# Optimization experiments

Measured on AMD Instinct MI355X. Metric: run time of the kernel, lower is better.

## Reference

```python
import jax, jax.numpy as jnp
import numpy as np

N, K, C, H, FF, OUT = 50000, 48, 128, 8, 256, 128
D = C // H  # head dim


def layernorm(x, g, b, eps=1e-5):
    m = jnp.mean(x, axis=-1, keepdims=True)
    v = jnp.mean((x - m) ** 2, axis=-1, keepdims=True)
    return (x - m) * jax.lax.rsqrt(v + eps) * g + b


def setup_inputs() -> dict:
    key = jax.random.key(0)
    ks = jax.random.split(key, 16)
    voxel_features = jax.random.normal(ks[0], (N, C), jnp.float32)
    voxel_coords = jax.random.uniform(ks[1], (N, 3), jnp.float32) * 400.0
    # neighbor indices; values >= N emulate missing neighbors (gather idx < 0 in original)
    raw = jax.random.randint(ks[2], (N, K), 0, N + N // 4)
    key_mask = raw >= N
    key_indices = jnp.where(key_mask, 0, raw).astype(jnp.int32)
    key_indices = key_indices.at[:, 0].set(jnp.arange(N, dtype=jnp.int32))  # self always valid
    key_mask = key_mask.at[:, 0].set(False)
    s = 1.0 / np.sqrt(C)
    params = dict(
        in_proj_w=jax.random.normal(ks[3], (3 * C, C), jnp.float32) * s,
        in_proj_b=jnp.zeros((3 * C,), jnp.float32),
        out_proj_w=jax.random.normal(ks[4], (C, C), jnp.float32) * s,
        out_proj_b=jnp.zeros((C,), jnp.float32),
        k_pos_w=jax.random.normal(ks[5], (C, 3), jnp.float32) * 0.5,
        k_pos_b=jnp.zeros((C,), jnp.float32),
        ln1_g=jnp.ones((C,), jnp.float32), ln1_b=jnp.zeros((C,), jnp.float32),
        ln2_g=jnp.ones((C,), jnp.float32), ln2_b=jnp.zeros((C,), jnp.float32),
        ff1_w=jax.random.normal(ks[6], (FF, C), jnp.float32) * s,
        ff1_b=jnp.zeros((FF,), jnp.float32),
        ff2_w=jax.random.normal(ks[7], (C, FF), jnp.float32) * (1.0 / np.sqrt(FF)),
        ff2_b=jnp.zeros((C,), jnp.float32),
        out_w=jax.random.normal(ks[8], (OUT, C), jnp.float32) * s,
        out_b=jnp.zeros((OUT,), jnp.float32),
        ln3_g=jnp.ones((OUT,), jnp.float32), ln3_b=jnp.zeros((OUT,), jnp.float32),
    )
    return dict(voxel_features=voxel_features, voxel_coords=voxel_coords,
                key_indices=key_indices, key_mask=key_mask, **params)


def reference(voxel_features, voxel_coords, key_indices, key_mask,
              in_proj_w, in_proj_b, out_proj_w, out_proj_b,
              k_pos_w, k_pos_b, ln1_g, ln1_b, ln2_g, ln2_b,
              ff1_w, ff1_b, ff2_w, ff2_b, out_w, out_b, ln3_g, ln3_b):
    # gather neighbor features and coords: [N, K, C] / [N, K, 3]
    key_feats = voxel_features[key_indices]
    rel_coords = voxel_coords[key_indices] - voxel_coords[:, None, :]
    # conv1d(3->C, kernel 1) + ReLU positional embedding
    pos_emb = jax.nn.relu(jnp.einsum('nkt,ct->nkc', rel_coords, k_pos_w) + k_pos_b)
    key_feats = key_feats + pos_emb
    # multi-head attention, query seq_len = 1 per voxel
    wq, wk, wv = in_proj_w[:C], in_proj_w[C:2 * C], in_proj_w[2 * C:]
    bq, bk, bv = in_proj_b[:C], in_proj_b[C:2 * C], in_proj_b[2 * C:]
    q = (voxel_features @ wq.T + bq).reshape(N, H, D)
    k = (jnp.einsum('nkc,ec->nke', key_feats, wk) + bk).reshape(N, K, H, D)
    v = (jnp.einsum('nkc,ec->nke', key_feats, wv) + bv).reshape(N, K, H, D)
    scores = jnp.einsum('nhd,nkhd->nhk', q, k) / np.sqrt(D)
    scores = jnp.where(key_mask[:, None, :], jnp.float32(-1e9), scores)
    attn = jax.nn.softmax(scores, axis=-1)
    ctx = jnp.einsum('nhk,nkhd->nhd', attn, v).reshape(N, C)
    attend = ctx @ out_proj_w.T + out_proj_b
    # residual + norm + FFN + norm
    x = layernorm(voxel_features + attend, ln1_g, ln1_b)
    ff = jax.nn.relu(x @ ff1_w.T + ff1_b) @ ff2_w.T + ff2_b
    x = layernorm(x + ff, ln2_g, ln2_b)
    # output layer: Linear -> LayerNorm -> ReLU
    out = jax.nn.relu(layernorm(x @ out_w.T + out_b, ln3_g, ln3_b))
    return out
```

## Files before the change

kernel.cpp:

```cpp
#include <hip/hip_runtime.h>
#include <stdint.h>

typedef unsigned char u8;
typedef unsigned short us;
typedef unsigned int u32;

#define CDIM  128
#define KNBR  48
#define HEADS 8
#define DHEAD 16
#define FFDIM 256

using bf16x8 = __attribute__((ext_vector_type(8))) short;
using f32x4  = __attribute__((ext_vector_type(4))) float;

__device__ inline float blo32(u32 u) { union { u32 i; float f; } v; v.i = u << 16; return v.f; }
__device__ inline float bhi32(u32 u) { union { u32 i; float f; } v; v.i = u & 0xFFFF0000u; return v.f; }
__device__ inline float bf2f(us u) { union { u32 i; float f; } v; v.i = ((u32)u) << 16; return v.f; }
__device__ inline us f2bf(float x) {
    union { float f; u32 i; } v; v.f = x;
    u32 r = v.i + 0x7FFFu + ((v.i >> 16) & 1u);
    return (us)(r >> 16);
}
__device__ inline u32 cvtpk(float a, float b) {
    u32 r;
    asm("v_cvt_pk_bf16_f32 %0, %1, %2" : "=v"(r) : "v"(a), "v"(b));
    return r;
}

__global__ void k_mask_probe(const u32* __restrict__ mw, int nwords,
                             int* __restrict__ flag)
{
    u32 any = 0;
    for (int j = blockIdx.x * blockDim.x + threadIdx.x; j < nwords;
         j += gridDim.x * blockDim.x)
        any |= mw[j] & 0xFFFFFF00u;
    if (any) atomicOr(flag, 1);
}

__global__ __launch_bounds__(256) void k_wt(
    const float* __restrict__ W, float* __restrict__ WT, int E, int C4)
{
    int i = blockIdx.x * 256 + threadIdx.x;
    if (i < E * C4) {
        int e = i / C4, c4 = i - e * C4;
        float4 v = *(const float4*)(W + (size_t)e * (C4 * 4) + c4 * 4);
        ((float4*)WT)[(size_t)c4 * E + e] = v;
    }
}

__global__ __launch_bounds__(256) void k_wb(
    const float* __restrict__ W, us* __restrict__ WB, int n2)
{
    int i = blockIdx.x * 256 + threadIdx.x;
    if (i < n2) {
        float2 v = *(const float2*)(W + (size_t)i * 2);
        ((u32*)WB)[i] = cvtpk(v.x, v.y);
    }
}

__global__ __launch_bounds__(384) void k_qkv(
    const float* __restrict__ F, const float* __restrict__ WT,
    const float* __restrict__ B,
    float* __restrict__ Q, us* __restrict__ FkB, us* __restrict__ FvB, int N)
{
    __shared__ float xL[8][CDIM];
    int row0 = blockIdx.x * 8;
    int t = threadIdx.x;
    for (int o = t; o < 8 * CDIM; o += 384) {
        int r = o >> 7, c = o & 127;
        int row = row0 + r;
        xL[r][c] = (row < N) ? F[row * CDIM + c] : 0.f;
    }
    __syncthreads();

    int e = t;
    const float4* WT4 = (const float4*)WT;
    float acc[8] = {0.f,0.f,0.f,0.f,0.f,0.f,0.f,0.f};
    #pragma unroll 8
    for (int c4 = 0; c4 < CDIM / 4; ++c4) {
        float4 w = WT4[c4 * 384 + e];
        #pragma unroll
        for (int r = 0; r < 8; ++r) {
            const float* x = &xL[r][c4 * 4];
            acc[r] += x[0]*w.x + x[1]*w.y + x[2]*w.z + x[3]*w.w;
        }
    }
    float bv = B[e];
    if (e < 128) {
        #pragma unroll
        for (int r = 0; r < 8; ++r) {
            int row = row0 + r;
            if (row < N) Q[row * CDIM + e] = acc[r] + bv;
        }
    } else if (e < 256) {
        int eo = e - 128;
        #pragma unroll
        for (int r = 0; r < 8; ++r) {
            int row = row0 + r;
            if (row < N) FkB[(size_t)row * CDIM + eo] = f2bf(acc[r] + bv);
        }
    } else {
        int eo = e - 256;
        #pragma unroll
        for (int r = 0; r < 8; ++r) {
            int row = row0 + r;
            if (row < N) FvB[(size_t)row * CDIM + eo] = f2bf(acc[r] + bv);
        }
    }
}

__global__ __launch_bounds__(256, 6) void k_attn(
    const float* __restrict__ coords, const int* __restrict__ kidx,
    const u8* __restrict__ kmask_u8, const int* __restrict__ kmask_i32,
    const int* __restrict__ maskflag,
    const float* __restrict__ Q, const us* __restrict__ FkB,
    const us* __restrict__ FvB,
    const float* __restrict__ wk, const float* __restrict__ wv,
    const float* __restrict__ kpw, const float* __restrict__ kpb,
    float* __restrict__ CTX)
{
    __shared__ __align__(16) u8 SM[14656];
    us*    qwH   = (us*)(SM);
    us*    qwL   = (us*)(SM + 2176);
    float* scL   = (float*)(SM + 4352);
    float* Ql    = (float*)(SM + 6016);
    float* rel   = (float*)(SM + 6528);
    float* kpw0S = (float*)(SM + 7104);
    float* kpw1S = (float*)(SM + 7616);
    float* kpw2S = (float*)(SM + 8128);
    float* kpbS  = (float*)(SM + 8640);
    int*   idxl  = (int*)  (SM + 9152);
    u8*    mskl  = (u8*)   (SM + 9344);
    float* Pb    = (float*)(SM + 9408);
    float* pc    = (float*)(SM + 13632);

    int n = blockIdx.x;
    int t = threadIdx.x;
    int w = t >> 6, lane = t & 63;

    if (t < KNBR) {
        int idx = kidx[n * KNBR + t];
        idxl[t] = idx;
        mskl[t] = maskflag[0] ? kmask_u8[n * KNBR + t]
                              : (u8)kmask_i32[n * KNBR + t];
        rel[t * 3 + 0] = coords[idx * 3 + 0] - coords[n * 3 + 0];
        rel[t * 3 + 1] = coords[idx * 3 + 1] - coords[n * 3 + 1];
        rel[t * 3 + 2] = coords[idx * 3 + 2] - coords[n * 3 + 2];
    }
    if (t < 128) {
        kpw0S[t] = kpw[t * 3 + 0];
        kpw1S[t] = kpw[t * 3 + 1];
        kpw2S[t] = kpw[t * 3 + 2];
        kpbS[t]  = kpb[t];
    } else {
        Ql[t - 128] = Q[n * CDIM + (t - 128)];
    }
    __syncthreads();

    {
        int h = t >> 5, c4 = t & 31;
        const float* qh = Ql + h * DHEAD;
        float a0=0.f, a1=0.f, a2=0.f, a3=0.f;
        #pragma unroll
        for (int d = 0; d < DHEAD; ++d) {
            float q = qh[d];
            float4 wr = *(const float4*)(wk + (size_t)(h * DHEAD + d) * CDIM + c4 * 4);
            a0 += q * wr.x; a1 += q * wr.y; a2 += q * wr.z; a3 += q * wr.w;
        }
        uint2 ph, pl;
        ph.x = cvtpk(a0, a1);
        ph.y = cvtpk(a2, a3);
        pl.x = cvtpk(a0 - blo32(ph.x), a1 - bhi32(ph.x));
        pl.y = cvtpk(a2 - blo32(ph.y), a3 - bhi32(ph.y));
        *(uint2*)&qwH[h * 136 + c4 * 4] = ph;
        *(uint2*)&qwL[h * 136 + c4 * 4] = pl;
    }

    if (w == 3) {
        #pragma unroll
        for (int i = 0; i < 6; ++i) {
            int o = lane * 6 + i;
            int k = o >> 3, h = o & 7;
            const float* qh = Ql + h * DHEAD;
            const uint4* fk = (const uint4*)(FkB + (size_t)idxl[k] * CDIM + h * DHEAD);
            uint4 fa = fk[0], fb = fk[1];
            float s = qh[0]*blo32(fa.x) + qh[1]*bhi32(fa.x)
                    + qh[2]*blo32(fa.y) + qh[3]*bhi32(fa.y)
                    + qh[4]*blo32(fa.z) + qh[5]*bhi32(fa.z)
                    + qh[6]*blo32(fa.w) + qh[7]*bhi32(fa.w)
                    + qh[8]*blo32(fb.x) + qh[9]*bhi32(fb.x)
                    + qh[10]*blo32(fb.y) + qh[11]*bhi32(fb.y)
                    + qh[12]*blo32(fb.z) + qh[13]*bhi32(fb.z)
                    + qh[14]*blo32(fb.w) + qh[15]*bhi32(fb.w);
            scL[h * 52 + k] = s;
        }
    }
    __syncthreads();

    union U8 { bf16x8 v; u32 wd[4]; };

    if (w < 3) {
        f32x4 acc = {0.f, 0.f, 0.f, 0.f};
        int kk = w * 16 + (lane & 15);
        int cb0 = (lane >> 4) * 8;
        int arow = lane & 15;
        bool aval = arow < 8;
        bf16x8 zz = {0,0,0,0,0,0,0,0};
        float r0 = rel[kk * 3], r1 = rel[kk * 3 + 1], r2 = rel[kk * 3 + 2];
        #pragma unroll
        for (int s = 0; s < 4; ++s) {
            int cb = cb0 + s * 32;
            float4 x0 = *(const float4*)&kpw0S[cb], x1 = *(const float4*)&kpw0S[cb + 4];
            float4 y0 = *(const float4*)&kpw1S[cb], y1 = *(const float4*)&kpw1S[cb + 4];
            float4 z0 = *(const float4*)&kpw2S[cb], z1 = *(const float4*)&kpw2S[cb + 4];
            float4 b0 = *(const float4*)&kpbS[cb],  b1 = *(const float4*)&kpbS[cb + 4];
            float p[8];
            p[0] = fmaxf(b0.x + r0*x0.x + r1*y0.x + r2*z0.x, 0.f);
            p[1] = fmaxf(b0.y + r0*x0.y + r1*y0.y + r2*z0.y, 0.f);
            p[2] = fmaxf(b0.z + r0*x0.z + r1*y0.z + r2*z0.z, 0.f);
            p[3] = fmaxf(b0.w + r0*x0.w + r1*y0.w + r2*z0.w, 0.f);
            p[4] = fmaxf(b1.x + r0*x1.x + r1*y1.x + r2*z1.x, 0.f);
            p[5] = fmaxf(b1.y + r0*x1.y + r1*y1.y + r2*z1.y, 0.f);
            p[6] = fmaxf(b1.z + r0*x1.z + r1*y1.z + r2*z1.z, 0.f);
            p[7] = fmaxf(b1.w + r0*x1.w + r1*y1.w + r2*z1.w, 0.f);
            U8 bh, bl;
            #pragma unroll
            for (int j = 0; j < 4; ++j) {
                u32 hh = cvtpk(p[2*j], p[2*j+1]);
                bh.wd[j] = hh;
                bl.wd[j] = cvtpk(p[2*j] - blo32(hh), p[2*j+1] - bhi32(hh));
            }
            int c0 = s * 32 + cb0;
            bf16x8 ah = aval ? *(const bf16x8*)(qwH + arow * 136 + c0) : zz;
            bf16x8 al = aval ? *(const bf16x8*)(qwL + arow * 136 + c0) : zz;
            acc = __builtin_amdgcn_mfma_f32_16x16x32_bf16(ah, bh.v, acc, 0, 0, 0);
            acc = __builtin_amdgcn_mfma_f32_16x16x32_bf16(ah, bl.v, acc, 0, 0, 0);
            acc = __builtin_amdgcn_mfma_f32_16x16x32_bf16(al, bh.v, acc, 0, 0, 0);
        }
        if (lane < 32) {
            int kc = w * 16 + (lane & 15);
            int rb = (lane >> 4) * 4;
            u8 mk = mskl[kc];
            #pragma unroll
            for (int j = 0; j < 4; ++j) {
                int h = rb + j;
                float s = acc[j] + scL[h * 52 + kc];
                scL[h * 52 + kc] = mk ? -1e30f : s * 0.25f;
            }
        }
    }
    __syncthreads();

    {
        int h = t >> 5, l32 = t & 31;
        float* sc = scL + h * 52;
        float v0 = sc[l32];
        float v1 = (l32 < KNBR - 32) ? sc[l32 + 32] : -1e30f;
        float m = fmaxf(v0, v1);
        #pragma unroll
        for (int off = 16; off >= 1; off >>= 1)
            m = fmaxf(m, __shfl_xor(m, off, 32));
        float e0 = __expf(v0 - m);
        float e1 = (l32 < KNBR - 32) ? __expf(v1 - m) : 0.f;
        float s = e0 + e1;
        #pragma unroll
        for (int off = 16; off >= 1; off >>= 1)
            s += __shfl_xor(s, off, 32);
        float inv = 1.f / s;
        sc[l32] = e0 * inv;
        if (l32 < KNBR - 32) sc[l32 + 32] = e1 * inv;
    }
    __syncthreads();

    {
        bf16x8 AH[2], AL[2];
        int arow = lane & 15;
        bool av = arow < 8;
        #pragma unroll
        for (int st = 0; st < 2; ++st) {
            int k0 = (lane >> 4) * 8 + st * 32;
            float pr[8];
            if (av && k0 < KNBR) {
                float4 s0 = *(const float4*)&scL[arow * 52 + k0];
                float4 s1 = *(const float4*)&scL[arow * 52 + k0 + 4];
                pr[0]=s0.x; pr[1]=s0.y; pr[2]=s0.z; pr[3]=s0.w;
                pr[4]=s1.x; pr[5]=s1.y; pr[6]=s1.z; pr[7]=s1.w;
            } else {
                #pragma unroll
                for (int j = 0; j < 8; ++j) pr[j] = 0.f;
            }
            U8 ah, al;
            #pragma unroll
            for (int j = 0; j < 4; ++j) {
                u32 hh = cvtpk(pr[2*j], pr[2*j+1]);
                ah.wd[j] = hh;
                al.wd[j] = cvtpk(pr[2*j] - blo32(hh), pr[2*j+1] - bhi32(hh));
            }
            AH[st] = ah.v; AL[st] = al.v;
        }
        #pragma unroll
        for (int ct = 0; ct < 2; ++ct) {
            int c = w * 32 + ct * 16 + (lane & 15);
            float w0 = kpw0S[c], w1 = kpw1S[c], w2 = kpw2S[c], bb = kpbS[c];
            f32x4 acc = {0.f, 0.f, 0.f, 0.f};
            #pragma unroll
            for (int st = 0; st < 2; ++st) {
                int k0 = (lane >> 4) * 8 + st * 32;
                U8 bh;
                if (k0 < KNBR) {
                    #pragma unroll
                    for (int j = 0; j < 4; ++j) {
                        const float* ra = rel + (k0 + 2*j) * 3;
                        const float* rb = rel + (k0 + 2*j + 1) * 3;
                        float pa = fmaxf(bb + ra[0]*w0 + ra[1]*w1 + ra[2]*w2, 0.f);
                        float pb = fmaxf(bb + rb[0]*w0 + rb[1]*w1 + rb[2]*w2, 0.f);
                        bh.wd[j] = cvtpk(pa, pb);
                    }
                } else {
                    bh.wd[0]=bh.wd[1]=bh.wd[2]=bh.wd[3]=0u;
                }
                acc = __builtin_amdgcn_mfma_f32_16x16x32_bf16(AH[st], bh.v, acc, 0, 0, 0);
                acc = __builtin_amdgcn_mfma_f32_16x16x32_bf16(AL[st], bh.v, acc, 0, 0, 0);
            }
            if (lane < 32) {
                int rb2 = (lane >> 4) * 4;
                #pragma unroll
                for (int j = 0; j < 4; ++j)
                    Pb[(rb2 + j) * 132 + c] = acc[j];
            }
        }
    }
    __syncthreads();

    {
        int c = t & 127, half = t >> 7;
        int h = c >> 4;
        const float* sc = scL + h * 52;
        float accF = 0.f;
        #pragma unroll 4
        for (int kk = 0; kk < 24; ++kk) {
            int k = half * 24 + kk;
            accF += sc[k] * bf2f(FvB[(size_t)idxl[k] * CDIM + c]);
        }
        const float4* wr = (const float4*)(wv + (size_t)c * CDIM) + half * 16;
        const float4* pb4 = (const float4*)(Pb + h * 132) + half * 16;
        #pragma unroll 4
        for (int j = 0; j < 16; ++j) {
            float4 wq = wr[j], p = pb4[j];
            accF += wq.x*p.x + wq.y*p.y + wq.z*p.z + wq.w*p.w;
        }
        pc[half * 128 + c] = accF;
    }
    __syncthreads();
    if (t < CDIM) CTX[n * CDIM + t] = pc[t] + pc[128 + t];
}

__global__ __launch_bounds__(256) void k_proj_ln_m(
    const float* __restrict__ X, const float* __restrict__ RES,
    const us* __restrict__ WB, const float* __restrict__ B,
    const float* __restrict__ G, const float* __restrict__ LB,
    float* __restrict__ OUT, int N, int relu_out)
{
    __shared__ us xB[16 * 136];
    __shared__ float aL[16][CDIM + 4];
    __shared__ float mu[16], rs[16];
    int row0 = blockIdx.x * 16;
    int t = threadIdx.x;
    {
        int r = t >> 4, cb = (t & 15) * 8;
        int row = row0 + r;
        uint4 o = make_uint4(0, 0, 0, 0);
        if (row < N) {
            float4 v0 = *(const float4*)&X[(size_t)row * CDIM + cb];
            float4 v1 = *(const float4*)&X[(size_t)row * CDIM + cb + 4];
            o.x = cvtpk(v0.x, v0.y); o.y = cvtpk(v0.z, v0.w);
            o.z = cvtpk(v1.x, v1.y); o.w = cvtpk(v1.z, v1.w);
        }
        *(uint4*)&xB[r * 136 + cb] = o;
    }
    __syncthreads();

    int w = t >> 6, lane = t & 63;
    int arow = lane & 15, ko = (lane >> 4) * 8;
    bf16x8 afr[4];
    #pragma unroll
    for (int s = 0; s < 4; ++s)
        afr[s] = *(const bf16x8*)&xB[arow * 136 + s * 32 + ko];

    #pragma unroll
    for (int ct = 0; ct < 2; ++ct) {
        int e0 = (w * 2 + ct) * 16;
        f32x4 acc = {0.f, 0.f, 0.f, 0.f};
        #pragma unroll
        for (int s = 0; s < 4; ++s) {
            bf16x8 bfr = *(const bf16x8*)&WB[(size_t)(e0 + arow) * CDIM + s * 32 + ko];
            acc = __builtin_amdgcn_mfma_f32_16x16x32_bf16(afr[s], bfr, acc, 0, 0, 0);
        }
        int e = e0 + arow;
        float bb = B[e];
        #pragma unroll
        for (int jj = 0; jj < 4; ++jj) {
            int r = (lane >> 4) * 4 + jj;
            int row = row0 + r;
            float a = acc[jj] + bb;
            if (RES != nullptr && row < N) a += RES[(size_t)row * CDIM + e];
            aL[r][e] = a;
        }
    }
    __syncthreads();

    {
        int r = t >> 4, j = t & 15;
        float s = 0.f;
        #pragma unroll
        for (int jj = 0; jj < 8; ++jj) s += aL[r][j * 8 + jj];
        #pragma unroll
        for (int off = 8; off >= 1; off >>= 1) s += __shfl_xor(s, off, 16);
        float mean = s * (1.f / 128.f);
        float v = 0.f;
        #pragma unroll
        for (int jj = 0; jj < 8; ++jj) {
            float d = aL[r][j * 8 + jj] - mean; v += d * d;
        }
        #pragma unroll
        for (int off = 8; off >= 1; off >>= 1) v += __shfl_xor(v, off, 16);
        if (j == 0) { mu[r] = mean; rs[r] = rsqrtf(v * (1.f / 128.f) + 1e-5f); }
    }
    __syncthreads();

    for (int o = t; o < 16 * CDIM; o += 256) {
        int r = o >> 7, c = o & 127;
        int row = row0 + r;
        if (row < N) {
            float y = (aL[r][c] - mu[r]) * rs[r] * G[c] + LB[c];
            if (relu_out) y = fmaxf(y, 0.f);
            OUT[row * CDIM + c] = y;
        }
    }
}

__global__ __launch_bounds__(256) void k_ff1_m(
    const float* __restrict__ X, const us* __restrict__ WB,
    const float* __restrict__ B, us* __restrict__ HID, int N)
{
    __shared__ us xB[16 * 136];
    int row0 = blockIdx.x * 16;
    int t = threadIdx.x;
    {
        int r = t >> 4, cb = (t & 15) * 8;
        int row = row0 + r;
        uint4 o = make_uint4(0, 0, 0, 0);
        if (row < N) {
            float4 v0 = *(const float4*)&X[(size_t)row * CDIM + cb];
            float4 v1 = *(const float4*)&X[(size_t)row * CDIM + cb + 4];
            o.x = cvtpk(v0.x, v0.y); o.y = cvtpk(v0.z, v0.w);
            o.z = cvtpk(v1.x, v1.y); o.w = cvtpk(v1.z, v1.w);
        }
        *(uint4*)&xB[r * 136 + cb] = o;
    }
    __syncthreads();

    int w = t >> 6, lane = t & 63;
    int arow = lane & 15, ko = (lane >> 4) * 8;
    bf16x8 afr[4];
    #pragma unroll
    for (int s = 0; s < 4; ++s)
        afr[s] = *(const bf16x8*)&xB[arow * 136 + s * 32 + ko];

    #pragma unroll
    for (int ct = 0; ct < 4; ++ct) {
        int e0 = (w * 4 + ct) * 16;
        f32x4 acc = {0.f, 0.f, 0.f, 0.f};
        #pragma unroll
        for (int s = 0; s < 4; ++s) {
            bf16x8 bfr = *(const bf16x8*)&WB[(size_t)(e0 + arow) * CDIM + s * 32 + ko];
            acc = __builtin_amdgcn_mfma_f32_16x16x32_bf16(afr[s], bfr, acc, 0, 0, 0);
        }
        int e = e0 + arow;
        float bb = B[e];
        #pragma unroll
        for (int jj = 0; jj < 4; ++jj) {
            int r = (lane >> 4) * 4 + jj;
            int row = row0 + r;
            if (row < N)
                HID[(size_t)row * FFDIM + e] = f2bf(fmaxf(acc[jj] + bb, 0.f));
        }
    }
}

__global__ __launch_bounds__(256) void k_ff2_ln_m(
    const us* __restrict__ HID, const float* __restrict__ RES,
    const us* __restrict__ WB, const float* __restrict__ B,
    const float* __restrict__ G, const float* __restrict__ LB,
    float* __restrict__ OUT, int N)
{
    __shared__ us xB[16 * 264];
    __shared__ float aL[16][CDIM + 4];
    __shared__ float mu[16], rs[16];
    int row0 = blockIdx.x * 16;
    int t = threadIdx.x;
    {
        int r = t >> 4, cb = (t & 15) * 16;
        int row = row0 + r;
        uint4 o0 = make_uint4(0,0,0,0), o1 = make_uint4(0,0,0,0);
        if (row < N) {
            const uint4* hp = (const uint4*)&HID[(size_t)row * FFDIM + cb];
            o0 = hp[0]; o1 = hp[1];
        }
        *(uint4*)&xB[r * 264 + cb] = o0;
        *(uint4*)&xB[r * 264 + cb + 8] = o1;
    }
    __syncthreads();

    int w = t >> 6, lane = t & 63;
    int arow = lane & 15, ko = (lane >> 4) * 8;
    #pragma unroll
    for (int ct = 0; ct < 2; ++ct) {
        int e0 = (w * 2 + ct) * 16;
        f32x4 acc = {0.f, 0.f, 0.f, 0.f};
        #pragma unroll
        for (int s = 0; s < 8; ++s) {
            bf16x8 af = *(const bf16x8*)&xB[arow * 264 + s * 32 + ko];
            bf16x8 bfr = *(const bf16x8*)&WB[(size_t)(e0 + arow) * FFDIM + s * 32 + ko];
            acc = __builtin_amdgcn_mfma_f32_16x16x32_bf16(af, bfr, acc, 0, 0, 0);
        }
        int e = e0 + arow;
        float bb = B[e];
        #pragma unroll
        for (int jj = 0; jj < 4; ++jj) {
            int r = (lane >> 4) * 4 + jj;
            int row = row0 + r;
            float a = acc[jj] + bb;
            if (row < N) a += RES[(size_t)row * CDIM + e];
            aL[r][e] = a;
        }
    }
    __syncthreads();

    {
        int r = t >> 4, j = t & 15;
        float s = 0.f;
        #pragma unroll
        for (int jj = 0; jj < 8; ++jj) s += aL[r][j * 8 + jj];
        #pragma unroll
        for (int off = 8; off >= 1; off >>= 1) s += __shfl_xor(s, off, 16);
        float mean = s * (1.f / 128.f);
        float v = 0.f;
        #pragma unroll
        for (int jj = 0; jj < 8; ++jj) {
            float d = aL[r][j * 8 + jj] - mean; v += d * d;
        }
        #pragma unroll
        for (int off = 8; off >= 1; off >>= 1) v += __shfl_xor(v, off, 16);
        if (j == 0) { mu[r] = mean; rs[r] = rsqrtf(v * (1.f / 128.f) + 1e-5f); }
    }
    __syncthreads();

    for (int o = t; o < 16 * CDIM; o += 256) {
        int r = o >> 7, c = o & 127;
        int row = row0 + r;
        if (row < N)
            OUT[row * CDIM + c] = (aL[r][c] - mu[r]) * rs[r] * G[c] + LB[c];
    }
}

extern "C" void kernel_launch(void* const* d_in, const int* in_sizes, int n_in,
                              void* d_out, int out_size, void* d_ws, size_t ws_size,
                              hipStream_t stream)
{
    const float* F      = (const float*)d_in[0];
    const float* coords = (const float*)d_in[1];
    const int*   kidx   = (const int*)d_in[2];
    const void*  kmask  = d_in[3];
    const float* ipw    = (const float*)d_in[4];
    const float* ipb    = (const float*)d_in[5];
    const float* opw    = (const float*)d_in[6];
    const float* opb    = (const float*)d_in[7];
    const float* kpw    = (const float*)d_in[8];
    const float* kpb    = (const float*)d_in[9];
    const float* ln1g   = (const float*)d_in[10];
    const float* ln1b   = (const float*)d_in[11];
    const float* ln2g   = (const float*)d_in[12];
    const float* ln2b   = (const float*)d_in[13];
    const float* w1     = (const float*)d_in[14];
    const float* b1     = (const float*)d_in[15];
    const float* w2     = (const float*)d_in[16];
    const float* b2     = (const float*)d_in[17];
    const float* ow     = (const float*)d_in[18];
    const float* ob     = (const float*)d_in[19];
    const float* ln3g   = (const float*)d_in[20];
    const float* ln3b   = (const float*)d_in[21];

    int N = in_sizes[0] / CDIM;
    size_t NC = (size_t)N * CDIM;

    float* ws  = (float*)d_ws;
    float* Q    = ws;
    us*    FkB  = (us*)(ws + NC);
    us*    FvB  = (us*)(ws + NC) + NC;
    float* CTX  = ws + 2 * NC;
    float* X1   = Q;
    us*    HID  = (us*)(ws + NC);
    float* X2   = ws + 3 * NC;
    float* WTq  = ws + 4 * NC;
    us*    WBo  = (us*)(WTq + 384 * 128);
    us*    WB1  = WBo + 128 * 128;
    us*    WB2  = WB1 + 256 * 128;
    us*    WBw  = WB2 + 128 * 256;
    int*   mflag = (int*)(WBw + 128 * 128);

    const float* wk = ipw + CDIM * CDIM;
    const float* wv = ipw + 2 * CDIM * CDIM;

    hipMemsetAsync(mflag, 0, sizeof(int), stream);
    int nwords = (N * KNBR) / 4;
    k_mask_probe<<<256, 256, 0, stream>>>((const u32*)kmask, nwords, mflag);

    k_wt<<<(384 * 32 + 255) / 256, 256, 0, stream>>>(ipw, WTq, 384, 32);
    k_wb<<<(128 * 64 + 255) / 256, 256, 0, stream>>>(opw, WBo, 128 * 64);
    k_wb<<<(256 * 64 + 255) / 256, 256, 0, stream>>>(w1,  WB1, 256 * 64);
    k_wb<<<(128 * 128 + 255) / 256, 256, 0, stream>>>(w2, WB2, 128 * 128);
    k_wb<<<(128 * 64 + 255) / 256, 256, 0, stream>>>(ow,  WBw, 128 * 64);

    k_qkv<<<(N + 7) / 8, 384, 0, stream>>>(F, WTq, ipb, Q, FkB, FvB, N);
    k_attn<<<N, 256, 0, stream>>>(coords, kidx, (const u8*)kmask,
                                  (const int*)kmask, mflag, Q, FkB, FvB,
                                  wk, wv, kpw, kpb, CTX);
    k_proj_ln_m<<<(N + 15) / 16, 256, 0, stream>>>(CTX, F, WBo, opb,
                                                   ln1g, ln1b, X1, N, 0);
    k_ff1_m<<<(N + 15) / 16, 256, 0, stream>>>(X1, WB1, b1, HID, N);
    k_ff2_ln_m<<<(N + 15) / 16, 256, 0, stream>>>(HID, X1, WB2, b2,
                                                  ln2g, ln2b, X2, N);
    k_proj_ln_m<<<(N + 15) / 16, 256, 0, stream>>>(X2, nullptr, WBw, ob,
                                                   ln3g, ln3b, (float*)d_out, N, 1);
}
```

Measured before the change: 832.2 us.

## Compute QKV projection with bf16 MFMA using hi/lo split precision

Replaces the FP32 SIMT QKV projection with a matrix-core kernel. Inputs and the Q weights are split into bf16 high and low parts, giving three MFMAs for near-FP32 Q accuracy, while K/V use two MFMAs because their outputs are stored in bf16 anyway. The weight preprocessing changes from a transpose to bf16 hi/lo conversion. It aims to cut the projection's FP32 ALU cost, with a small risk to numerical accuracy of K/V.

```diff
diff --git a/kernel.cpp b/kernel.cpp
--- a/kernel.cpp
+++ b/kernel.cpp
@@ -38,17 +38,6 @@
     if (any) atomicOr(flag, 1);
 }
 
-__global__ __launch_bounds__(256) void k_wt(
-    const float* __restrict__ W, float* __restrict__ WT, int E, int C4)
-{
-    int i = blockIdx.x * 256 + threadIdx.x;
-    if (i < E * C4) {
-        int e = i / C4, c4 = i - e * C4;
-        float4 v = *(const float4*)(W + (size_t)e * (C4 * 4) + c4 * 4);
-        ((float4*)WT)[(size_t)c4 * E + e] = v;
-    }
-}
-
 __global__ __launch_bounds__(256) void k_wb(
     const float* __restrict__ W, us* __restrict__ WB, int n2)
 {
@@ -59,53 +48,93 @@
     }
 }
 
-__global__ __launch_bounds__(384) void k_qkv(
-    const float* __restrict__ F, const float* __restrict__ WT,
-    const float* __restrict__ B,
+__global__ __launch_bounds__(256) void k_wb_hl(
+    const float* __restrict__ W, us* __restrict__ WH, us* __restrict__ WL,
+    int n2)
+{
+    int i = blockIdx.x * 256 + threadIdx.x;
+    if (i < n2) {
+        float2 v = *(const float2*)(W + (size_t)i * 2);
+        u32 h = cvtpk(v.x, v.y);
+        ((u32*)WH)[i] = h;
+        ((u32*)WL)[i] = cvtpk(v.x - blo32(h), v.y - bhi32(h));
+    }
+}
+
+__global__ __launch_bounds__(256) void k_qkv_m(
+    const float* __restrict__ F,
+    const us* __restrict__ WQh, const us* __restrict__ WQl,
+    const us* __restrict__ WKV, const float* __restrict__ B,
     float* __restrict__ Q, us* __restrict__ FkB, us* __restrict__ FvB, int N)
 {
-    __shared__ float xL[8][CDIM];
-    int row0 = blockIdx.x * 8;
+    __shared__ us xH[16 * 136];
+    __shared__ us xLo[16 * 136];
+    int row0 = blockIdx.x * 16;
     int t = threadIdx.x;
-    for (int o = t; o < 8 * CDIM; o += 384) {
-        int r = o >> 7, c = o & 127;
+    {
+        int r = t >> 4, cb = (t & 15) * 8;
         int row = row0 + r;
-        xL[r][c] = (row < N) ? F[row * CDIM + c] : 0.f;
-    }
-    __syncthreads();
-
-    int e = t;
-    const float4* WT4 = (const float4*)WT;
-    float acc[8] = {0.f,0.f,0.f,0.f,0.f,0.f,0.f,0.f};
-    #pragma unroll 8
-    for (int c4 = 0; c4 < CDIM / 4; ++c4) {
-        float4 w = WT4[c4 * 384 + e];
-        #pragma unroll
-        for (int r = 0; r < 8; ++r) {
-            const float* x = &xL[r][c4 * 4];
-            acc[r] += x[0]*w.x + x[1]*w.y + x[2]*w.z + x[3]*w.w;
-        }
-    }
-    float bv = B[e];
-    if (e < 128) {
-        #pragma unroll
-        for (int r = 0; r < 8; ++r) {
+        uint4 oh = make_uint4(0,0,0,0), ol = make_uint4(0,0,0,0);
+        if (row < N) {
+            float4 v0 = *(const float4*)&F[(size_t)row * CDIM + cb];
+            float4 v1 = *(const float4*)&F[(size_t)row * CDIM + cb + 4];
+            oh.x = cvtpk(v0.x, v0.y); oh.y = cvtpk(v0.z, v0.w);
+            oh.z = cvtpk(v1.x, v1.y); oh.w = cvtpk(v1.z, v1.w);
+            ol.x = cvtpk(v0.x - blo32(oh.x), v0.y - bhi32(oh.x));
+            ol.y = cvtpk(v0.z - blo32(oh.y), v0.w - bhi32(oh.y));
+            ol.z = cvtpk(v1.x - blo32(oh.z), v1.y - bhi32(oh.z));
+            ol.w = cvtpk(v1.z - blo32(oh.w), v1.w - bhi32(oh.w));
+        }
+        *(uint4*)&xH[r * 136 + cb] = oh;
+        *(uint4*)&xLo[r * 136 + cb] = ol;
+    }
+    __syncthreads();
+
+    int w = t >> 6, lane = t & 63;
+    int arow = lane & 15, ko = (lane >> 4) * 8;
+    bf16x8 ah[4], al[4];
+    #pragma unroll
+    for (int s = 0; s < 4; ++s) {
+        ah[s] = *(const bf16x8*)&xH[arow * 136 + s * 32 + ko];
+        al[s] = *(const bf16x8*)&xLo[arow * 136 + s * 32 + ko];
+    }
+
+    #pragma unroll
+    for (int i = 0; i < 6; ++i) {
+        int tile = w + 4 * i;
+        int e0 = tile * 16;
+        f32x4 acc = {0.f, 0.f, 0.f, 0.f};
+        if (tile < 8) {
+            const us* wh = WQh + (size_t)(e0 + arow) * CDIM;
+            const us* wl = WQl + (size_t)(e0 + arow) * CDIM;
+            #pragma unroll
+            for (int s = 0; s < 4; ++s) {
+                bf16x8 bh = *(const bf16x8*)(wh + s * 32 + ko);
+                bf16x8 bl = *(const bf16x8*)(wl + s * 32 + ko);
+                acc = __builtin_amdgcn_mfma_f32_16x16x32_bf16(ah[s], bh, acc, 0, 0, 0);
+                acc = __builtin_amdgcn_mfma_f32_16x16x32_bf16(ah[s], bl, acc, 0, 0, 0);
+                acc = __builtin_amdgcn_mfma_f32_16x16x32_bf16(al[s], bh, acc, 0, 0, 0);
+            }
+        } else {
+            const us* wp = WKV + (size_t)(e0 - 128 + arow) * CDIM;
+            #pragma unroll
+            for (int s = 0; s < 4; ++s) {
+                bf16x8 bh = *(const bf16x8*)(wp + s * 32 + ko);
+                acc = __builtin_amdgcn_mfma_f32_16x16x32_bf16(ah[s], bh, acc, 0, 0, 0);
+                acc = __builtin_amdgcn_mfma_f32_16x16x32_bf16(al[s], bh, acc, 0, 0, 0);
+            }
+        }
+        int e = e0 + arow;
+        float bb = B[e];
+        #pragma unroll
+        for (int jj = 0; jj < 4; ++jj) {
+            int r = (lane >> 4) * 4 + jj;
             int row = row0 + r;
-            if (row < N) Q[row * CDIM + e] = acc[r] + bv;
-        }
-    } else if (e < 256) {
-        int eo = e - 128;
-        #pragma unroll
-        for (int r = 0; r < 8; ++r) {
-            int row = row0 + r;
-            if (row < N) FkB[(size_t)row * CDIM + eo] = f2bf(acc[r] + bv);
-        }
-    } else {
-        int eo = e - 256;
-        #pragma unroll
-        for (int r = 0; r < 8; ++r) {
-            int row = row0 + r;
-            if (row < N) FvB[(size_t)row * CDIM + eo] = f2bf(acc[r] + bv);
+            if (row >= N) continue;
+            float a = acc[jj] + bb;
+            if (e < 128)       Q[(size_t)row * CDIM + e] = a;
+            else if (e < 256)  FkB[(size_t)row * CDIM + (e - 128)] = f2bf(a);
+            else               FvB[(size_t)row * CDIM + (e - 256)] = f2bf(a);
         }
     }
 }
@@ -232,11 +261,11 @@
                 bl.wd[j] = cvtpk(p[2*j] - blo32(hh), p[2*j+1] - bhi32(hh));
             }
             int c0 = s * 32 + cb0;
-            bf16x8 ah = aval ? *(const bf16x8*)(qwH + arow * 136 + c0) : zz;
-            bf16x8 al = aval ? *(const bf16x8*)(qwL + arow * 136 + c0) : zz;
-            acc = __builtin_amdgcn_mfma_f32_16x16x32_bf16(ah, bh.v, acc, 0, 0, 0);
-            acc = __builtin_amdgcn_mfma_f32_16x16x32_bf16(ah, bl.v, acc, 0, 0, 0);
-            acc = __builtin_amdgcn_mfma_f32_16x16x32_bf16(al, bh.v, acc, 0, 0, 0);
+            bf16x8 ahf = aval ? *(const bf16x8*)(qwH + arow * 136 + c0) : zz;
+            bf16x8 alf = aval ? *(const bf16x8*)(qwL + arow * 136 + c0) : zz;
+            acc = __builtin_amdgcn_mfma_f32_16x16x32_bf16(ahf, bh.v, acc, 0, 0, 0);
+            acc = __builtin_amdgcn_mfma_f32_16x16x32_bf16(ahf, bl.v, acc, 0, 0, 0);
+            acc = __builtin_amdgcn_mfma_f32_16x16x32_bf16(alf, bh.v, acc, 0, 0, 0);
         }
         if (lane < 32) {
             int kc = w * 16 + (lane & 15);
@@ -603,8 +632,10 @@
     float* X1   = Q;
     us*    HID  = (us*)(ws + NC);
     float* X2   = ws + 3 * NC;
-    float* WTq  = ws + 4 * NC;
-    us*    WBo  = (us*)(WTq + 384 * 128);
+    us*    WQh  = (us*)(ws + 4 * NC);
+    us*    WQl  = WQh + 128 * 128;
+    us*    WKV  = WQl + 128 * 128;
+    us*    WBo  = WKV + 256 * 128;
     us*    WB1  = WBo + 128 * 128;
     us*    WB2  = WB1 + 256 * 128;
     us*    WBw  = WB2 + 128 * 256;
@@ -617,13 +648,15 @@
     int nwords = (N * KNBR) / 4;
     k_mask_probe<<<256, 256, 0, stream>>>((const u32*)kmask, nwords, mflag);
 
-    k_wt<<<(384 * 32 + 255) / 256, 256, 0, stream>>>(ipw, WTq, 384, 32);
+    k_wb_hl<<<(128 * 64 + 255) / 256, 256, 0, stream>>>(ipw, WQh, WQl, 128 * 64);
+    k_wb<<<(256 * 64 + 255) / 256, 256, 0, stream>>>(ipw + 128 * CDIM, WKV, 256 * 64);
     k_wb<<<(128 * 64 + 255) / 256, 256, 0, stream>>>(opw, WBo, 128 * 64);
     k_wb<<<(256 * 64 + 255) / 256, 256, 0, stream>>>(w1,  WB1, 256 * 64);
     k_wb<<<(128 * 128 + 255) / 256, 256, 0, stream>>>(w2, WB2, 128 * 128);
     k_wb<<<(128 * 64 + 255) / 256, 256, 0, stream>>>(ow,  WBw, 128 * 64);
 
-    k_qkv<<<(N + 7) / 8, 384, 0, stream>>>(F, WTq, ipb, Q, FkB, FvB, N);
+    k_qkv_m<<<(N + 15) / 16, 256, 0, stream>>>(F, WQh, WQl, WKV, ipb,
+                                               Q, FkB, FvB, N);
     k_attn<<<N, 256, 0, stream>>>(coords, kidx, (const u8*)kmask,
                                   (const int*)kmask, mflag, Q, FkB, FvB,
                                   wk, wv, kpw, kpb, CTX);
```

After: 777.0 us. 1.07x faster.
